# Performance work log

Measured on AMD Instinct MI355X. Metric: run time of the kernel, lower is better.

Reference implementation:

```python
import jax, jax.numpy as jnp
import numpy as np

D_MODEL = 4096
D_HIDDEN = 32768
BATCH = 2048
K = 128
N_DEAD = 2048


def _ln(x, eps=1e-5):
    # torch .std() is unbiased (ddof=1)
    mu = jnp.mean(x, axis=-1, keepdims=True)
    xc = x - mu
    std = jnp.std(x, axis=-1, keepdims=True, ddof=1)
    return xc / (std + eps), mu, std


def _topk_activation(x, k):
    # topk over last dim, relu values, scatter back into zeros
    vals, idx = jax.lax.top_k(x, k)          # [B, k]
    vals = jax.nn.relu(vals)
    rows = jnp.arange(x.shape[0])[:, None]    # [B, 1]
    return jnp.zeros_like(x).at[rows, idx].set(vals)


def setup_inputs() -> dict:
    key = jax.random.key(0)
    k1, k2 = jax.random.split(key)
    x = jax.random.normal(k1, (BATCH, D_MODEL), dtype=jnp.float32)
    # kaiming-uniform-ish encoder init
    bound = 1.0 / np.sqrt(D_MODEL)
    w_enc = jax.random.uniform(k2, (D_MODEL, D_HIDDEN), dtype=jnp.float32,
                               minval=-bound, maxval=bound)
    w_dec = w_enc.T
    w_dec = w_dec / jnp.linalg.norm(w_dec, axis=0, keepdims=True)
    b_enc = jnp.zeros((D_HIDDEN,), dtype=jnp.float32)
    b_pre = jnp.zeros((D_MODEL,), dtype=jnp.float32)
    # fixed dead-neuron mask with exactly N_DEAD dead latents
    dm = np.zeros((D_HIDDEN,), dtype=bool)
    rng = np.random.default_rng(0)
    dm[rng.choice(D_HIDDEN, size=N_DEAD, replace=False)] = True
    dead_mask = jnp.asarray(dm)
    return {"x": x, "w_enc": w_enc, "w_dec": w_dec, "b_enc": b_enc,
            "b_pre": b_pre, "dead_mask": dead_mask, "num_dead": N_DEAD}


def reference(x, w_enc, w_dec, b_enc, b_pre, dead_mask, num_dead):
    xn, mu, std = _ln(x)
    xc = xn - b_pre
    pre_acts = xc @ w_enc + b_enc                 # [B, d_hidden]
    latents = _topk_activation(pre_acts, K)
    recons = latents @ w_dec + b_pre              # [B, d_model]
    recons = recons * std + mu
    # auxk dead-neuron path (num_dead is a static python int)
    k_aux = min(x.shape[-1] // 2, num_dead)
    auxk_latents = jnp.where(dead_mask[None, :], pre_acts, -jnp.inf)
    auxk_acts = _topk_activation(auxk_latents, k_aux)
    auxk = auxk_acts @ w_dec + b_pre
    auxk = auxk * std + mu
    return recons, auxk, num_dead
```

## Files before the change

### kernel.cpp

```cpp
#include <hip/hip_runtime.h>
#include <math.h>

#define D_MODEL  4096
#define D_HIDDEN 32768
#define BATCH    2048
#define KSEL     128
#define NDEAD    2048
#define TIECAP   256

#define NB_SEL 2048
#define NB_AG  2048
#define NB_AB  8192
#define NB_WD  8192

typedef short s16x8 __attribute__((ext_vector_type(8)));
typedef float f32x4 __attribute__((ext_vector_type(4)));

__device__ __forceinline__ unsigned int fkey(float f) {
    unsigned int u = __float_as_uint(f);
    return (u & 0x80000000u) ? ~u : (u | 0x80000000u);
}
__device__ __forceinline__ unsigned short f2bf(float f) {
    unsigned int u = __float_as_uint(f);
    u += 0x7FFFu + ((u >> 16) & 1u);
    return (unsigned short)(u >> 16);
}
__device__ __forceinline__ float bf2f(unsigned short h) {
    return __uint_as_float(((unsigned int)h) << 16);
}
__device__ __forceinline__ unsigned int key16x2(unsigned int u) {
    const unsigned int s = (u >> 15) & 0x10001u;
    const unsigned int mask = s * 0xFFFFu;
    return (u ^ mask) | (~mask & 0x80008000u);
}
__device__ __forceinline__ float unkey16(unsigned int k) {
    const unsigned int u = (k & 0x8000u) ? (k & 0x7FFFu) : (~k & 0xFFFFu);
    return __uint_as_float(u << 16);
}
__device__ __forceinline__ void async_copy16(void* lds_dst, const void* gsrc) {
    __builtin_amdgcn_global_load_lds(
        (const __attribute__((address_space(1))) unsigned int*)gsrc,
        (__attribute__((address_space(3))) unsigned int*)lds_dst,
        16, 0, 0);
}

__global__ __launch_bounds__(256) void prep_kernel(
    const float* __restrict__ x, const float* __restrict__ b_pre,
    double* __restrict__ mu, double* __restrict__ stdv, double* __restrict__ sinv,
    unsigned short* __restrict__ Ahp, float* __restrict__ xch, float* __restrict__ xcl,
    const unsigned char* __restrict__ mask8, int* __restrict__ dead_idx,
    int* __restrict__ dead_cnt, const int* __restrict__ num_dead_in,
    float* __restrict__ out_last)
{
    const int row = blockIdx.x;
    const int tid = threadIdx.x;
    if (row == BATCH) {
        if (tid >= 64) return;
        const int lane = tid;
        int c = 0;
        for (int j = lane; j < D_HIDDEN; j += 64) c += (mask8[j] != 0);
#pragma unroll
        for (int off = 32; off > 0; off >>= 1) c += __shfl_down(c, off, 64);
        const int total_u8 = __shfl(c, 0, 64);
        const bool u8mode = (total_u8 == NDEAD);
        const int* mask32 = (const int*)mask8;
        int cnt = 0;
        for (int base = 0; base < D_HIDDEN; base += 64) {
            const int j = base + lane;
            const bool d = u8mode ? (mask8[j] != 0) : (mask32[j] != 0);
            const unsigned long long b = __ballot(d);
            const int pre = __popcll(b & ((1ull << lane) - 1ull));
            if (d && (cnt + pre) < NDEAD) dead_idx[cnt + pre] = j;
            cnt += __popcll(b);
        }
        const int cc = cnt > NDEAD ? NDEAD : cnt;
        if (lane == 0) {
            *dead_cnt = cc;
            *out_last = (float)(*num_dead_in);
        }
        for (int t = cc + lane; t < NDEAD; t += 64) dead_idx[t] = 0;
        return;
    }
    const float* xr = x + (size_t)row * D_MODEL;
    float xv[16];
#pragma unroll
    for (int i = 0; i < 16; ++i) xv[i] = xr[tid + 256 * i];
    double s = 0.0;
#pragma unroll
    for (int i = 0; i < 16; ++i) s += (double)xv[i];
    __shared__ double red[4];
    __shared__ double sh_mu, sh_si;
    const int lane = tid & 63, wid = tid >> 6;
#pragma unroll
    for (int off = 32; off > 0; off >>= 1) s += __shfl_down(s, off, 64);
    if (lane == 0) red[wid] = s;
    __syncthreads();
    if (tid == 0) sh_mu = (red[0] + red[1] + red[2] + red[3]) / (double)D_MODEL;
    __syncthreads();
    const double m = sh_mu;
    double s2 = 0.0;
#pragma unroll
    for (int i = 0; i < 16; ++i) { double d = (double)xv[i] - m; s2 += d * d; }
#pragma unroll
    for (int off = 32; off > 0; off >>= 1) s2 += __shfl_down(s2, off, 64);
    __syncthreads();
    if (lane == 0) red[wid] = s2;
    __syncthreads();
    if (tid == 0) {
        double var = (red[0] + red[1] + red[2] + red[3]) / (double)(D_MODEL - 1);
        double sd = sqrt(var);
        mu[row] = m;
        stdv[row] = sd;
        const double si = 1.0 / (sd + 1e-5);
        sinv[row] = si;
        sh_si = si;
    }
    __syncthreads();
    const double si = sh_si;
#pragma unroll
    for (int i = 0; i < 4; ++i) {
        const int j = (i * 256 + tid) * 4;
        const float4 x4 = *(const float4*)(xr + j);
        const float4 bp = *(const float4*)(b_pre + j);
        float vf[4], hi[4], lo[4];
        const float xe[4] = {x4.x, x4.y, x4.z, x4.w};
        const float be[4] = {bp.x, bp.y, bp.z, bp.w};
#pragma unroll
        for (int e = 0; e < 4; ++e) {
            const double t = ((double)xe[e] - m) * si;
            vf[e] = (float)t - be[e];
            const double a = t - (double)be[e];
            hi[e] = (float)a;
            lo[e] = (float)(a - (double)hi[e]);
        }
        uint2 hw;
        hw.x = (unsigned)f2bf(vf[0]) | ((unsigned)f2bf(vf[1]) << 16);
        hw.y = (unsigned)f2bf(vf[2]) | ((unsigned)f2bf(vf[3]) << 16);
        *(uint2*)(Ahp + (size_t)row * D_MODEL + j) = hw;
        *(float4*)(xch + (size_t)row * D_MODEL + j) = make_float4(hi[0], hi[1], hi[2], hi[3]);
        *(float4*)(xcl + (size_t)row * D_MODEL + j) = make_float4(lo[0], lo[1], lo[2], lo[3]);
    }
}

__global__ __launch_bounds__(256) void bsplit_kernel(
    const float* __restrict__ w_enc, unsigned short* __restrict__ Bhp)
{
    __shared__ float t[32][33];
    const int bk = blockIdx.x * 32;
    const int bn = blockIdx.y * 32;
    const int tid = threadIdx.x;
    const int lr = tid >> 3, lc4 = (tid & 7) * 4;
    const float4 v = *(const float4*)(w_enc + (size_t)(bk + lr) * D_HIDDEN + bn + lc4);
    t[lr][lc4 + 0] = v.x; t[lr][lc4 + 1] = v.y; t[lr][lc4 + 2] = v.z; t[lr][lc4 + 3] = v.w;
    __syncthreads();
    float o[4];
#pragma unroll
    for (int j = 0; j < 4; ++j) o[j] = t[lc4 + j][lr];
    uint2 hw;
    hw.x = (unsigned)f2bf(o[0]) | ((unsigned)f2bf(o[1]) << 16);
    hw.y = (unsigned)f2bf(o[2]) | ((unsigned)f2bf(o[3]) << 16);
    *(uint2*)(Bhp + (size_t)(bn + lr) * D_MODEL + bk + lc4) = hw;
}

__global__ __launch_bounds__(256) void wencT_kernel(
    const float* __restrict__ w_enc, float* __restrict__ wT)
{
    __shared__ float t[32][33];
    const int bk = blockIdx.x * 32;
    const int bn = blockIdx.y * 32;
    const int tid = threadIdx.x;
    const int lr = tid >> 3, lc4 = (tid & 7) * 4;
    const float4 v = *(const float4*)(w_enc + (size_t)(bk + lr) * D_HIDDEN + bn + lc4);
    t[lr][lc4 + 0] = v.x; t[lr][lc4 + 1] = v.y; t[lr][lc4 + 2] = v.z; t[lr][lc4 + 3] = v.w;
    __syncthreads();
    const int j = tid >> 3, i4 = (tid & 7) * 4;
    float4 o;
    o.x = t[i4 + 0][j]; o.y = t[i4 + 1][j]; o.z = t[i4 + 2][j]; o.w = t[i4 + 3][j];
    *(float4*)(wT + (size_t)(bn + j) * D_MODEL + bk + i4) = o;
}

__global__ __launch_bounds__(256) void wprep_kernel(
    const float* __restrict__ w_enc, unsigned short* __restrict__ Bhp,
    float* __restrict__ wT)
{
    __shared__ float t[32][33];
    const int bk = blockIdx.x * 32;
    const int bn = blockIdx.y * 32;
    const int tid = threadIdx.x;
    const int lr = tid >> 3, lc4 = (tid & 7) * 4;
    const float4 v = *(const float4*)(w_enc + (size_t)(bk + lr) * D_HIDDEN + bn + lc4);
    t[lr][lc4 + 0] = v.x; t[lr][lc4 + 1] = v.y; t[lr][lc4 + 2] = v.z; t[lr][lc4 + 3] = v.w;
    __syncthreads();
    float o[4];
#pragma unroll
    for (int j = 0; j < 4; ++j) o[j] = t[lc4 + j][lr];
    uint2 hw;
    hw.x = (unsigned)f2bf(o[0]) | ((unsigned)f2bf(o[1]) << 16);
    hw.y = (unsigned)f2bf(o[2]) | ((unsigned)f2bf(o[3]) << 16);
    *(uint2*)(Bhp + (size_t)(bn + lr) * D_MODEL + bk + lc4) = hw;
    *(float4*)(wT + (size_t)(bn + lr) * D_MODEL + bk + lc4) = make_float4(o[0], o[1], o[2], o[3]);
}

template<int EPI>
__global__ __launch_bounds__(512) void mm256_kernel(
    const unsigned short* __restrict__ A, const unsigned short* __restrict__ B,
    const int kdim, const int ntiles_x,
    const float* __restrict__ bias_n,
    const double* __restrict__ muv, const double* __restrict__ stdvv,
    void* __restrict__ outp, const long ostride)
{
    __shared__ unsigned short lds[2 * 4 * 8192];
    const int tid = threadIdx.x;
    const int lane = tid & 63, wid = tid >> 6;
    const int cpx = gridDim.x >> 3;
    const int orig = blockIdx.x;
    const int wg = (orig & 7) * cpx + (orig >> 3);
    const int m0 = (wg % ntiles_x) * 256;
    const int n0 = (wg / ntiles_x) * 256;
    const int wm = (wid >> 2) * 128;
    const int wn = (wid & 3) * 64;
    const int fr = lane & 15, kq = lane >> 4;
    const int swr = (fr >> 1) & 3;
    const int qg = (lane & 3) ^ ((lane >> 3) & 3);
    const int qo = (kq ^ swr) * 8;

    f32x4 acc[8][4];
#pragma unroll
    for (int i = 0; i < 8; ++i)
#pragma unroll
        for (int j = 0; j < 4; ++j) acc[i][j] = (f32x4){0.f, 0.f, 0.f, 0.f};

    const unsigned short* sH0[4];
    int dH0[4];
#pragma unroll
    for (int j = 0; j < 4; ++j) {
        const int g = wid * 4 + j;
        const int is_b = g >> 4;
        const int sr = g & 15;
        const unsigned short* gp = is_b ? B : A;
        const int t0 = is_b ? n0 : m0;
        sH0[j] = gp + (size_t)(t0 + sr * 16 + (lane >> 2)) * kdim + qg * 8;
        dH0[j] = (is_b ? 2 : 0) * 8192 + sr * 512;
    }

    const int NT = kdim >> 6;
#pragma unroll
    for (int j = 0; j < 4; ++j) async_copy16(lds + dH0[j], sH0[j]);
#pragma unroll
    for (int j = 0; j < 4; ++j) async_copy16(lds + 8192 + dH0[j], sH0[j] + 32);
    if (NT > 1) {
#pragma unroll
        for (int j = 0; j < 4; ++j) async_copy16(lds + 32768 + dH0[j], sH0[j] + 64);
    }

    for (int t = 0; t < NT; ++t) {
        const int cur = t & 1;
        unsigned short* bb = (unsigned short*)lds + cur * 32768;
        unsigned short* nb = (unsigned short*)lds + (cur ^ 1) * 32768;
        const int k1 = (t + 1) << 6;
        const int k2 = (t + 2) << 6;

        if (t < NT - 1) { asm volatile("s_waitcnt vmcnt(8)" ::: "memory"); }
        else            { asm volatile("s_waitcnt vmcnt(4)" ::: "memory"); }
        asm volatile("s_barrier" ::: "memory");
        __builtin_amdgcn_sched_barrier(0);
        {
            if (t + 1 < NT) {
                async_copy16(nb + 8192 + dH0[0], sH0[0] + k1 + 32);
                async_copy16(nb + 8192 + dH0[1], sH0[1] + k1 + 32);
            }
            s16x8 a[4], b[4];
#pragma unroll
            for (int mi = 0; mi < 4; ++mi)
                a[mi] = *(const s16x8*)(bb + (wm + mi * 16 + fr) * 32 + qo);
#pragma unroll
            for (int ni = 0; ni < 4; ++ni)
                b[ni] = *(const s16x8*)(bb + 2 * 8192 + (wn + ni * 16 + fr) * 32 + qo);
            __builtin_amdgcn_s_setprio(1);
#pragma unroll
            for (int mi = 0; mi < 4; ++mi)
#pragma unroll
                for (int ni = 0; ni < 4; ++ni)
                    acc[mi][ni] = __builtin_amdgcn_mfma_f32_16x16x32_bf16(a[mi], b[ni], acc[mi][ni], 0, 0, 0);
            __builtin_amdgcn_s_setprio(0);
            asm volatile("s_barrier" ::: "memory");
            __builtin_amdgcn_sched_barrier(0);
            if (t + 1 < NT) {
                async_copy16(nb + 8192 + dH0[2], sH0[2] + k1 + 32);
                async_copy16(nb + 8192 + dH0[3], sH0[3] + k1 + 32);
            }
            s16x8 a2[4];
#pragma unroll
            for (int mi = 0; mi < 4; ++mi)
                a2[mi] = *(const s16x8*)(bb + (wm + (mi + 4) * 16 + fr) * 32 + qo);
            __builtin_amdgcn_s_setprio(1);
#pragma unroll
            for (int mi = 0; mi < 4; ++mi)
#pragma unroll
                for (int ni = 0; ni < 4; ++ni)
                    acc[mi + 4][ni] = __builtin_amdgcn_mfma_f32_16x16x32_bf16(a2[mi], b[ni], acc[mi + 4][ni], 0, 0, 0);
            __builtin_amdgcn_s_setprio(0);
        }
        if (t < NT - 1) { asm volatile("s_waitcnt vmcnt(8)" ::: "memory"); }
        else            { asm volatile("s_waitcnt vmcnt(0)" ::: "memory"); }
        asm volatile("s_barrier" ::: "memory");
        __builtin_amdgcn_sched_barrier(0);
        {
            if (t + 2 < NT) {
                async_copy16(bb + dH0[0], sH0[0] + k2);
                async_copy16(bb + dH0[1], sH0[1] + k2);
            }
            s16x8 a[4], b[4];
#pragma unroll
            for (int mi = 0; mi < 4; ++mi)
                a[mi] = *(const s16x8*)(bb + 8192 + (wm + mi * 16 + fr) * 32 + qo);
#pragma unroll
            for (int ni = 0; ni < 4; ++ni)
                b[ni] = *(const s16x8*)(bb + 3 * 8192 + (wn + ni * 16 + fr) * 32 + qo);
            __builtin_amdgcn_s_setprio(1);
#pragma unroll
            for (int mi = 0; mi < 4; ++mi)
#pragma unroll
                for (int ni = 0; ni < 4; ++ni)
                    acc[mi][ni] = __builtin_amdgcn_mfma_f32_16x16x32_bf16(a[mi], b[ni], acc[mi][ni], 0, 0, 0);
            __builtin_amdgcn_s_setprio(0);
            asm volatile("s_barrier" ::: "memory");
            __builtin_amdgcn_sched_barrier(0);
            if (t + 2 < NT) {
                async_copy16(bb + dH0[2], sH0[2] + k2);
                async_copy16(bb + dH0[3], sH0[3] + k2);
            }
            s16x8 a2[4];
#pragma unroll
            for (int mi = 0; mi < 4; ++mi)
                a2[mi] = *(const s16x8*)(bb + 8192 + (wm + (mi + 4) * 16 + fr) * 32 + qo);
            __builtin_amdgcn_s_setprio(1);
#pragma unroll
            for (int mi = 0; mi < 4; ++mi)
#pragma unroll
                for (int ni = 0; ni < 4; ++ni)
                    acc[mi + 4][ni] = __builtin_amdgcn_mfma_f32_16x16x32_bf16(a2[mi], b[ni], acc[mi + 4][ni], 0, 0, 0);
            __builtin_amdgcn_s_setprio(0);
        }
    }

#pragma unroll
    for (int ni = 0; ni < 4; ++ni) {
        const int col = n0 + wn + ni * 16 + fr;
        const float be = bias_n[col];
#pragma unroll
        for (int mi = 0; mi < 8; ++mi) {
            const int rb = m0 + wm + mi * 16 + kq * 4;
            if (EPI == 0) {
                unsigned short* O = (unsigned short*)outp;
#pragma unroll
                for (int r = 0; r < 4; ++r)
                    O[(size_t)(rb + r) * ostride + col] = f2bf(acc[mi][ni][r] + be);
            } else {
                float* O = (float*)outp;
#pragma unroll
                for (int r = 0; r < 4; ++r) {
                    const int m = rb + r;
                    O[(size_t)m * ostride + col] =
                        (acc[mi][ni][r] + be) * (float)stdvv[m] + (float)muv[m];
                }
            }
        }
    }
}

__global__ __launch_bounds__(256) void comboA_kernel(
    const unsigned short* __restrict__ p16,
    int* __restrict__ topk_idx, float* __restrict__ topk_val,
    int* __restrict__ sure_cnt, int* __restrict__ tie_cnt, int* __restrict__ cand_col,
    const int* __restrict__ dead_idx, const int* __restrict__ dead_cnt,
    unsigned short* __restrict__ Ahd,
    const float* __restrict__ w_dec, unsigned short* __restrict__ Bhd,
    unsigned short* __restrict__ wd16,
    const int nb_ab, const int nb_wd)
{
    const int b = blockIdx.x;
    const int tid = threadIdx.x;
    __shared__ float tsm[32][33];
    __shared__ int red[4];
    __shared__ int sh_sel, sh_tie;

    if (b < NB_SEL) {
        const int row = b;
        const int lane = tid & 63, wid = tid >> 6;
        const unsigned short* pr = p16 + (size_t)row * D_HIDDEN;
        uint4 kr[16];
#pragma unroll
        for (int i = 0; i < 16; ++i) {
            uint4 w = *(const uint4*)(pr + (i * 256 + tid) * 8);
            w.x = key16x2(w.x); w.y = key16x2(w.y); w.z = key16x2(w.z); w.w = key16x2(w.w);
            kr[i] = w;
        }
        if (tid == 0) { sh_sel = 0; sh_tie = 0; }
        unsigned int lo = 0, hi = 65535;
        while (lo < hi) {
            const unsigned int mid = (lo + hi) >> 1;
            int c = 0;
#pragma unroll
            for (int i = 0; i < 16; ++i) {
                const unsigned int u[4] = {kr[i].x, kr[i].y, kr[i].z, kr[i].w};
#pragma unroll
                for (int e = 0; e < 4; ++e) {
                    c += (int)((u[e] & 0xFFFFu) > mid);
                    c += (int)((u[e] >> 16) > mid);
                }
            }
#pragma unroll
            for (int off = 32; off > 0; off >>= 1) c += __shfl_down(c, off, 64);
            if (lane == 0) red[wid] = c;
            __syncthreads();
            const int total = red[0] + red[1] + red[2] + red[3];
            if (total < KSEL) hi = mid; else lo = mid + 1;
            __syncthreads();
        }
        const unsigned int K16 = lo;
        const float vc = unkey16(K16);
        const float DLT = 1.3e-2f;
        const float sureT = vc + 2.f * DLT;
        const float candT = vc - 2.f * DLT;
        const unsigned int sK = fkey(sureT) >> 16;
        const unsigned int cK = fkey(candT) >> 16;
        int* oidx = topk_idx + row * KSEL;
        float* oval = topk_val + row * KSEL;
        int* cc = cand_col + row * TIECAP;
#pragma unroll
        for (int i = 0; i < 16; ++i) {
            const int j0 = (i * 256 + tid) * 8;
            const unsigned int u[4] = {kr[i].x, kr[i].y, kr[i].z, kr[i].w};
#pragma unroll
            for (int e = 0; e < 8; ++e) {
                const unsigned int k = (e & 1) ? (u[e >> 1] >> 16) : (u[e >> 1] & 0xFFFFu);
                if (k < cK) continue;
                const float v = unkey16(k);
                if (k > sK && v > sureT) {
                    const int pos = atomicAdd(&sh_sel, 1);
                    oidx[pos] = j0 + e;
                    oval[pos] = v > 0.f ? v : 0.f;
                } else if (v >= candT) {
                    const int t = atomicAdd(&sh_tie, 1);
                    if (t < TIECAP) cc[t] = j0 + e;
                }
            }
        }
        __syncthreads();
        if (tid == 0) {
            sure_cnt[row] = sh_sel;
            tie_cnt[row] = sh_tie > TIECAP ? TIECAP : sh_tie;
        }
        return;
    }
    if (b < NB_SEL + NB_AG) {
        const int r = b - NB_SEL;
        const int dc = *dead_cnt;
#pragma unroll
        for (int i = 0; i < 8; ++i) {
            const int c = i * 256 + tid;
            unsigned short v = 0;
            if (c < dc) {
                const unsigned short u = p16[(size_t)r * D_HIDDEN + dead_idx[c]];
                v = (u & 0x8000u) ? (unsigned short)0 : u;
            }
            Ahd[(size_t)r * NDEAD + c] = v;
        }
        return;
    }
    if (b < NB_SEL + NB_AG + nb_ab) {
        const int idx = b - (NB_SEL + NB_AG);
        const int k0 = (idx & 63) * 32;
        const int n0 = (idx >> 6) * 32;
        const int i = tid >> 3, j4 = (tid & 7) * 4;
        const int srow = dead_idx[k0 + i];
        const float4 v = *(const float4*)(w_dec + (size_t)srow * D_MODEL + n0 + j4);
        tsm[i][j4 + 0] = v.x; tsm[i][j4 + 1] = v.y; tsm[i][j4 + 2] = v.z; tsm[i][j4 + 3] = v.w;
        __syncthreads();
        const int j = tid >> 3, i4 = (tid & 7) * 4;
        uint2 hw;
        hw.x = (unsigned)f2bf(tsm[i4 + 0][j]) | ((unsigned)f2bf(tsm[i4 + 1][j]) << 16);
        hw.y = (unsigned)f2bf(tsm[i4 + 2][j]) | ((unsigned)f2bf(tsm[i4 + 3][j]) << 16);
        *(uint2*)(Bhd + (size_t)(n0 + j) * NDEAD + k0 + i4) = hw;
        return;
    }
    {
        const int bb = b - (NB_SEL + NB_AG + nb_ab);
        (void)nb_wd;
        const size_t base0 = (size_t)bb * 16384;
#pragma unroll
        for (int it = 0; it < 8; ++it) {
            const size_t off = base0 + (size_t)it * 2048 + (size_t)tid * 8;
            const float4 a = *(const float4*)(w_dec + off);
            const float4 c = *(const float4*)(w_dec + off + 4);
            uint4 o;
            o.x = (unsigned)f2bf(a.x) | ((unsigned)f2bf(a.y) << 16);
            o.y = (unsigned)f2bf(a.z) | ((unsigned)f2bf(a.w) << 16);
            o.z = (unsigned)f2bf(c.x) | ((unsigned)f2bf(c.y) << 16);
            o.w = (unsigned)f2bf(c.z) | ((unsigned)f2bf(c.w) << 16);
            *(uint4*)(wd16 + off) = o;
        }
        return;
    }
}

__global__ __launch_bounds__(256) void auxb_kernel(
    const float* __restrict__ w_dec, const int* __restrict__ dead_idx,
    unsigned short* __restrict__ Bhd)
{
    __shared__ float t[32][33];
    const int k0 = blockIdx.x * 32;
    const int n0 = blockIdx.y * 32;
    const int tid = threadIdx.x;
    const int i = tid >> 3, j4 = (tid & 7) * 4;
    const int srow = dead_idx[k0 + i];
    const float4 v = *(const float4*)(w_dec + (size_t)srow * D_MODEL + n0 + j4);
    t[i][j4 + 0] = v.x; t[i][j4 + 1] = v.y; t[i][j4 + 2] = v.z; t[i][j4 + 3] = v.w;
    __syncthreads();
    const int j = tid >> 3, i4 = (tid & 7) * 4;
    uint2 hw;
    hw.x = (unsigned)f2bf(t[i4 + 0][j]) | ((unsigned)f2bf(t[i4 + 1][j]) << 16);
    hw.y = (unsigned)f2bf(t[i4 + 2][j]) | ((unsigned)f2bf(t[i4 + 3][j]) << 16);
    *(uint2*)(Bhd + (size_t)(n0 + j) * NDEAD + k0 + i4) = hw;
}

__global__ __launch_bounds__(256) void wdec2bf_kernel(
    const float* __restrict__ w_dec, unsigned short* __restrict__ wd16)
{
    const size_t gid = (size_t)blockIdx.x * 256 + threadIdx.x;
    const size_t base = gid * 8;
    const float4 a = *(const float4*)(w_dec + base);
    const float4 b = *(const float4*)(w_dec + base + 4);
    uint4 o;
    o.x = (unsigned)f2bf(a.x) | ((unsigned)f2bf(a.y) << 16);
    o.y = (unsigned)f2bf(a.z) | ((unsigned)f2bf(a.w) << 16);
    o.z = (unsigned)f2bf(b.x) | ((unsigned)f2bf(b.y) << 16);
    o.w = (unsigned)f2bf(b.z) | ((unsigned)f2bf(b.w) << 16);
    *(uint4*)(wd16 + base) = o;
}

__global__ __launch_bounds__(256) void topk_refine_kernel(
    const int* __restrict__ tie_cnt, const int* __restrict__ cand_col,
    double* __restrict__ cand_val,
    const float* __restrict__ xch, const float* __restrict__ xcl,
    const float* __restrict__ wT, const float* __restrict__ b_enc)
{
    const int row = blockIdx.x;
    const int tid = threadIdx.x;
    const int lane = tid & 63, wid = tid >> 6;
    const int T = tie_cnt[row];
    const int base = (int)blockIdx.y * 4 + wid;
    if (base >= T) return;
    const float* hr = xch + (size_t)row * D_MODEL;
    const float* lr2 = xcl + (size_t)row * D_MODEL;
    for (int slot = base; slot < T; slot += 64) {
        const int col = cand_col[row * TIECAP + slot];
        const float* wr = wT + (size_t)col * D_MODEL;
        double s0 = 0.0, s1 = 0.0;
        for (int k = lane * 4; k < D_MODEL; k += 512) {
            {
                const float4 h = *(const float4*)(hr + k);
                const float4 l = *(const float4*)(lr2 + k);
                const float4 w4 = *(const float4*)(wr + k);
                s0 += ((double)h.x + (double)l.x) * (double)w4.x;
                s0 += ((double)h.y + (double)l.y) * (double)w4.y;
                s0 += ((double)h.z + (double)l.z) * (double)w4.z;
                s0 += ((double)h.w + (double)l.w) * (double)w4.w;
            }
            {
                const int k2 = k + 256;
                const float4 h = *(const float4*)(hr + k2);
                const float4 l = *(const float4*)(lr2 + k2);
                const float4 w4 = *(const float4*)(wr + k2);
                s1 += ((double)h.x + (double)l.x) * (double)w4.x;
                s1 += ((double)h.y + (double)l.y) * (double)w4.y;
                s1 += ((double)h.z + (double)l.z) * (double)w4.z;
                s1 += ((double)h.w + (double)l.w) * (double)w4.w;
            }
        }
        double s = s0 + s1;
#pragma unroll
        for (int off = 32; off > 0; off >>= 1) s += __shfl_down(s, off, 64);
        if (lane == 0) cand_val[row * TIECAP + slot] = s + (double)b_enc[col];
    }
}

__global__ __launch_bounds__(256) void decode_fin_kernel(
    const int* __restrict__ sure_cnt, const int* __restrict__ tie_cnt,
    const int* __restrict__ cand_col, const double* __restrict__ cand_val,
    const int* __restrict__ topk_idx, const float* __restrict__ topk_val,
    const unsigned short* __restrict__ wd16, const float* __restrict__ b_pre,
    const double* __restrict__ mu, const double* __restrict__ stdv,
    float* __restrict__ out0)
{
    const int row = blockIdx.x;
    const int tid = threadIdx.x;
    __shared__ double vals[TIECAP];
    __shared__ int cols[TIECAP];
    __shared__ int sidx[KSEL];
    __shared__ float sval[KSEL];
    const int G = sure_cnt[row];
    const int T = tie_cnt[row];
    const int R = KSEL - G;
    if (tid < T) {
        vals[tid] = cand_val[row * TIECAP + tid];
        cols[tid] = cand_col[row * TIECAP + tid];
    }
    if (tid < G) {
        sidx[tid] = topk_idx[row * KSEL + tid];
        sval[tid] = topk_val[row * KSEL + tid];
    }
    __syncthreads();
    if (tid < T) {
        const double v = vals[tid];
        const int c = cols[tid];
        int rank = 0;
        for (int u = 0; u < T; ++u) {
            const double vu = vals[u];
            rank += (int)((vu > v) || (vu == v && cols[u] < c));
        }
        if (rank < R) {
            sidx[G + rank] = c;
            sval[G + rank] = v > 0.0 ? (float)v : 0.f;
        }
    }
    const int take = R < T ? R : T;
    if (tid >= take && tid < R) {
        sidx[G + tid] = (T > 0) ? cols[0] : 0;
        sval[G + tid] = 0.f;
    }
    __syncthreads();
    float acc[16];
#pragma unroll
    for (int i = 0; i < 16; ++i) acc[i] = 0.f;
    const int dbase = tid * 16;
    for (int k = 0; k < KSEL; ++k) {
        const float v = sval[k];
        if (v == 0.f) continue;
        const uint4* wr = (const uint4*)(wd16 + (size_t)sidx[k] * D_MODEL + dbase);
        const uint4 w0 = wr[0], w1 = wr[1];
        const unsigned int u[8] = {w0.x, w0.y, w0.z, w0.w, w1.x, w1.y, w1.z, w1.w};
#pragma unroll
        for (int i = 0; i < 8; ++i) {
            acc[2 * i]     += v * __uint_as_float(u[i] << 16);
            acc[2 * i + 1] += v * __uint_as_float(u[i] & 0xFFFF0000u);
        }
    }
    const float st = (float)stdv[row];
    const float mm = (float)mu[row];
    float* o = out0 + (size_t)row * D_MODEL + dbase;
#pragma unroll
    for (int i = 0; i < 16; ++i) {
        o[i] = (acc[i] + b_pre[dbase + i]) * st + mm;
    }
}

extern "C" void kernel_launch(void* const* d_in, const int* in_sizes, int n_in,
                              void* d_out, int out_size, void* d_ws, size_t ws_size,
                              hipStream_t stream)
{
    (void)in_sizes; (void)n_in; (void)out_size;
    const float* x      = (const float*)d_in[0];
    const float* w_enc  = (const float*)d_in[1];
    const float* w_dec  = (const float*)d_in[2];
    const float* b_enc  = (const float*)d_in[3];
    const float* b_pre  = (const float*)d_in[4];
    const unsigned char* dead_mask = (const unsigned char*)d_in[5];
    const int* num_dead = (const int*)d_in[6];
    float* out = (float*)d_out;

    char* base = (char*)d_ws;
    char* w = base;
    auto alloc = [&](size_t bytes) -> char* {
        char* p = w;
        w += (bytes + 255) & ~(size_t)255;
        return p;
    };
    unsigned short* p16 = (unsigned short*)alloc((size_t)BATCH * D_HIDDEN * 2);
    double* mu       = (double*)alloc((size_t)BATCH * 8);
    double* stdv     = (double*)alloc((size_t)BATCH * 8);
    double* sinv     = (double*)alloc((size_t)BATCH * 8);
    int* topk_idx    = (int*)alloc((size_t)BATCH * KSEL * 4);
    float* topk_val  = (float*)alloc((size_t)BATCH * KSEL * 4);
    int* dead_idx    = (int*)alloc((size_t)NDEAD * 4);
    int* dead_cnt    = (int*)alloc(256);
    int* sure_cnt    = (int*)alloc((size_t)BATCH * 4);
    int* tie_cnt     = (int*)alloc((size_t)BATCH * 4);
    int* cand_col    = (int*)alloc((size_t)BATCH * TIECAP * 4);
    double* cand_val = (double*)alloc((size_t)BATCH * TIECAP * 8);
    float* xch       = (float*)alloc((size_t)BATCH * D_MODEL * 4);
    float* xcl       = (float*)alloc((size_t)BATCH * D_MODEL * 4);
    unsigned short* Ahp = (unsigned short*)alloc((size_t)BATCH * D_MODEL * 2);
    char* region     = alloc((size_t)D_HIDDEN * D_MODEL * 4);
    float* wT_big    = (float*)alloc((size_t)D_HIDDEN * D_MODEL * 4);
    const size_t need_big = (size_t)(w - base);
    const bool bigws = (ws_size >= need_big);

    unsigned short* Bhp = (unsigned short*)region;
    float* wT_small = (float*)region;
    unsigned short* wd16 = (unsigned short*)region;
    unsigned short* Bhd  = (unsigned short*)(region + (size_t)D_HIDDEN * D_MODEL * 2);
    unsigned short* Ahd  = Ahp;
    float* wT = bigws ? wT_big : wT_small;

    float* out0 = out;
    float* out1 = out + (size_t)BATCH * D_MODEL;
    float* out_last = out + (size_t)2 * BATCH * D_MODEL;

    prep_kernel<<<BATCH + 1, 256, 0, stream>>>(x, b_pre, mu, stdv, sinv, Ahp, xch, xcl,
                                               dead_mask, dead_idx, dead_cnt, num_dead, out_last);
    if (bigws) {
        wprep_kernel<<<dim3(D_MODEL / 32, D_HIDDEN / 32), 256, 0, stream>>>(w_enc, Bhp, wT);
    } else {
        bsplit_kernel<<<dim3(D_MODEL / 32, D_HIDDEN / 32), 256, 0, stream>>>(w_enc, Bhp);
    }
    mm256_kernel<0><<<(BATCH / 256) * (D_HIDDEN / 256), 512, 0, stream>>>(
        Ahp, Bhp, D_MODEL, BATCH / 256, b_enc, nullptr, nullptr, p16, (long)D_HIDDEN);
    if (bigws) {
        comboA_kernel<<<NB_SEL + NB_AG + NB_AB + NB_WD, 256, 0, stream>>>(
            p16, topk_idx, topk_val, sure_cnt, tie_cnt, cand_col,
            dead_idx, dead_cnt, Ahd, w_dec, Bhd, wd16, NB_AB, NB_WD);
        mm256_kernel<1><<<(BATCH / 256) * (D_MODEL / 256), 512, 0, stream>>>(
            Ahd, Bhd, NDEAD, BATCH / 256, b_pre, mu, stdv, out1, (long)D_MODEL);
        topk_refine_kernel<<<dim3(BATCH, 16), 256, 0, stream>>>(
            tie_cnt, cand_col, cand_val, xch, xcl, wT, b_enc);
    } else {
        wencT_kernel<<<dim3(D_MODEL / 32, D_HIDDEN / 32), 256, 0, stream>>>(w_enc, wT);
        comboA_kernel<<<NB_SEL + NB_AG, 256, 0, stream>>>(
            p16, topk_idx, topk_val, sure_cnt, tie_cnt, cand_col,
            dead_idx, dead_cnt, Ahd, w_dec, Bhd, wd16, 0, 0);
        topk_refine_kernel<<<dim3(BATCH, 16), 256, 0, stream>>>(
            tie_cnt, cand_col, cand_val, xch, xcl, wT, b_enc);
        auxb_kernel<<<dim3(NDEAD / 32, D_MODEL / 32), 256, 0, stream>>>(w_dec, dead_idx, Bhd);
        wdec2bf_kernel<<<(int)(((size_t)D_HIDDEN * D_MODEL) / (256 * 8)), 256, 0, stream>>>(w_dec, wd16);
        mm256_kernel<1><<<(BATCH / 256) * (D_MODEL / 256), 512, 0, stream>>>(
            Ahd, Bhd, NDEAD, BATCH / 256, b_pre, mu, stdv, out1, (long)D_MODEL);
    }
    decode_fin_kernel<<<BATCH, 256, 0, stream>>>(
        sure_cnt, tie_cnt, cand_col, cand_val, topk_idx, topk_val,
        wd16, b_pre, mu, stdv, out0);
}
```

Before: 2.069 ms.

## Fuse weight prep into LN prep, merge aux GEMM with top-k refine

Folds the w_enc transpose/bf16 conversion blocks into the layer-norm prep kernel as extra blocks. It also merges the aux-k decode GEMM and the tie-refinement dot products into one launch, comboB, with the GEMM tiles placed first. The refine path now runs one 512-thread block per row and stages the row's high/low activations in LDS, replacing the 16-way y-grid. The goal is fewer launches and overlap of small, unbalanced kernels, at the cost of lower refine parallelism per row and the heavy LDS footprint applying to all blocks.

```diff
diff --git a/kernel.cpp b/kernel.cpp
--- a/kernel.cpp
+++ b/kernel.cpp
@@ -12,6 +12,8 @@
 #define NB_AG  2048
 #define NB_AB  8192
 #define NB_WD  8192
+#define NB_MM  128
+#define NB_WPREP (128 * 1024)
 
 typedef short s16x8 __attribute__((ext_vector_type(8)));
 typedef float f32x4 __attribute__((ext_vector_type(4)));
@@ -44,17 +46,44 @@
         16, 0, 0);
 }
 
-__global__ __launch_bounds__(256) void prep_kernel(
+__global__ __launch_bounds__(256) void prepw_kernel(
     const float* __restrict__ x, const float* __restrict__ b_pre,
     double* __restrict__ mu, double* __restrict__ stdv, double* __restrict__ sinv,
     unsigned short* __restrict__ Ahp, float* __restrict__ xch, float* __restrict__ xcl,
     const unsigned char* __restrict__ mask8, int* __restrict__ dead_idx,
     int* __restrict__ dead_cnt, const int* __restrict__ num_dead_in,
-    float* __restrict__ out_last)
+    float* __restrict__ out_last,
+    const float* __restrict__ w_enc, unsigned short* __restrict__ Bhp,
+    float* __restrict__ wT, const int do_w)
 {
-    const int row = blockIdx.x;
+    const int b = blockIdx.x;
     const int tid = threadIdx.x;
-    if (row == BATCH) {
+    __shared__ double red[4];
+    __shared__ double sh_mu, sh_si;
+    __shared__ float tsm[32][33];
+
+    if (b > BATCH) {
+        const int wb = b - (BATCH + 1);
+        const int bk = (wb & 127) * 32;
+        const int bn = (wb >> 7) * 32;
+        const int lr = tid >> 3, lc4 = (tid & 7) * 4;
+        const float4 v = *(const float4*)(w_enc + (size_t)(bk + lr) * D_HIDDEN + bn + lc4);
+        tsm[lr][lc4 + 0] = v.x; tsm[lr][lc4 + 1] = v.y;
+        tsm[lr][lc4 + 2] = v.z; tsm[lr][lc4 + 3] = v.w;
+        __syncthreads();
+        float o[4];
+#pragma unroll
+        for (int j = 0; j < 4; ++j) o[j] = tsm[lc4 + j][lr];
+        uint2 hw;
+        hw.x = (unsigned)f2bf(o[0]) | ((unsigned)f2bf(o[1]) << 16);
+        hw.y = (unsigned)f2bf(o[2]) | ((unsigned)f2bf(o[3]) << 16);
+        *(uint2*)(Bhp + (size_t)(bn + lr) * D_MODEL + bk + lc4) = hw;
+        if (do_w)
+            *(float4*)(wT + (size_t)(bn + lr) * D_MODEL + bk + lc4) =
+                make_float4(o[0], o[1], o[2], o[3]);
+        return;
+    }
+    if (b == BATCH) {
         if (tid >= 64) return;
         const int lane = tid;
         int c = 0;
@@ -68,10 +97,10 @@
         for (int base = 0; base < D_HIDDEN; base += 64) {
             const int j = base + lane;
             const bool d = u8mode ? (mask8[j] != 0) : (mask32[j] != 0);
-            const unsigned long long b = __ballot(d);
-            const int pre = __popcll(b & ((1ull << lane) - 1ull));
+            const unsigned long long bm = __ballot(d);
+            const int pre = __popcll(bm & ((1ull << lane) - 1ull));
             if (d && (cnt + pre) < NDEAD) dead_idx[cnt + pre] = j;
-            cnt += __popcll(b);
+            cnt += __popcll(bm);
         }
         const int cc = cnt > NDEAD ? NDEAD : cnt;
         if (lane == 0) {
@@ -81,6 +110,7 @@
         for (int t = cc + lane; t < NDEAD; t += 64) dead_idx[t] = 0;
         return;
     }
+    const int row = b;
     const float* xr = x + (size_t)row * D_MODEL;
     float xv[16];
 #pragma unroll
@@ -88,8 +118,6 @@
     double s = 0.0;
 #pragma unroll
     for (int i = 0; i < 16; ++i) s += (double)xv[i];
-    __shared__ double red[4];
-    __shared__ double sh_mu, sh_si;
     const int lane = tid & 63, wid = tid >> 6;
 #pragma unroll
     for (int off = 32; off > 0; off >>= 1) s += __shfl_down(s, off, 64);
@@ -177,28 +205,6 @@
     float4 o;
     o.x = t[i4 + 0][j]; o.y = t[i4 + 1][j]; o.z = t[i4 + 2][j]; o.w = t[i4 + 3][j];
     *(float4*)(wT + (size_t)(bn + j) * D_MODEL + bk + i4) = o;
-}
-
-__global__ __launch_bounds__(256) void wprep_kernel(
-    const float* __restrict__ w_enc, unsigned short* __restrict__ Bhp,
-    float* __restrict__ wT)
-{
-    __shared__ float t[32][33];
-    const int bk = blockIdx.x * 32;
-    const int bn = blockIdx.y * 32;
-    const int tid = threadIdx.x;
-    const int lr = tid >> 3, lc4 = (tid & 7) * 4;
-    const float4 v = *(const float4*)(w_enc + (size_t)(bk + lr) * D_HIDDEN + bn + lc4);
-    t[lr][lc4 + 0] = v.x; t[lr][lc4 + 1] = v.y; t[lr][lc4 + 2] = v.z; t[lr][lc4 + 3] = v.w;
-    __syncthreads();
-    float o[4];
-#pragma unroll
-    for (int j = 0; j < 4; ++j) o[j] = t[lc4 + j][lr];
-    uint2 hw;
-    hw.x = (unsigned)f2bf(o[0]) | ((unsigned)f2bf(o[1]) << 16);
-    hw.y = (unsigned)f2bf(o[2]) | ((unsigned)f2bf(o[3]) << 16);
-    *(uint2*)(Bhp + (size_t)(bn + lr) * D_MODEL + bk + lc4) = hw;
-    *(float4*)(wT + (size_t)(bn + lr) * D_MODEL + bk + lc4) = make_float4(o[0], o[1], o[2], o[3]);
 }
 
 template<int EPI>
@@ -540,49 +546,218 @@
     *(uint4*)(wd16 + base) = o;
 }
 
-__global__ __launch_bounds__(256) void topk_refine_kernel(
+__global__ __launch_bounds__(512) void comboB_kernel(
+    const unsigned short* __restrict__ A, const unsigned short* __restrict__ B,
+    const float* __restrict__ bias_n,
+    const double* __restrict__ muv, const double* __restrict__ stdvv,
+    float* __restrict__ out1,
     const int* __restrict__ tie_cnt, const int* __restrict__ cand_col,
     double* __restrict__ cand_val,
     const float* __restrict__ xch, const float* __restrict__ xcl,
-    const float* __restrict__ wT, const float* __restrict__ b_enc)
+    const float* __restrict__ wT, const float* __restrict__ b_enc,
+    const int nb_mm)
 {
-    const int row = blockIdx.x;
+    __shared__ unsigned short lds[2 * 4 * 8192];
     const int tid = threadIdx.x;
     const int lane = tid & 63, wid = tid >> 6;
-    const int T = tie_cnt[row];
-    const int base = (int)blockIdx.y * 4 + wid;
-    if (base >= T) return;
-    const float* hr = xch + (size_t)row * D_MODEL;
-    const float* lr2 = xcl + (size_t)row * D_MODEL;
-    for (int slot = base; slot < T; slot += 64) {
-        const int col = cand_col[row * TIECAP + slot];
-        const float* wr = wT + (size_t)col * D_MODEL;
-        double s0 = 0.0, s1 = 0.0;
-        for (int k = lane * 4; k < D_MODEL; k += 512) {
-            {
-                const float4 h = *(const float4*)(hr + k);
-                const float4 l = *(const float4*)(lr2 + k);
-                const float4 w4 = *(const float4*)(wr + k);
-                s0 += ((double)h.x + (double)l.x) * (double)w4.x;
-                s0 += ((double)h.y + (double)l.y) * (double)w4.y;
-                s0 += ((double)h.z + (double)l.z) * (double)w4.z;
-                s0 += ((double)h.w + (double)l.w) * (double)w4.w;
-            }
-            {
-                const int k2 = k + 256;
-                const float4 h = *(const float4*)(hr + k2);
-                const float4 l = *(const float4*)(lr2 + k2);
-                const float4 w4 = *(const float4*)(wr + k2);
-                s1 += ((double)h.x + (double)l.x) * (double)w4.x;
-                s1 += ((double)h.y + (double)l.y) * (double)w4.y;
-                s1 += ((double)h.z + (double)l.z) * (double)w4.z;
-                s1 += ((double)h.w + (double)l.w) * (double)w4.w;
-            }
-        }
-        double s = s0 + s1;
-#pragma unroll
-        for (int off = 32; off > 0; off >>= 1) s += __shfl_down(s, off, 64);
-        if (lane == 0) cand_val[row * TIECAP + slot] = s + (double)b_enc[col];
+
+    if (blockIdx.x >= nb_mm) {
+        const int row = blockIdx.x - nb_mm;
+        const int T = tie_cnt[row];
+        if (T == 0) return;
+        float* shh = (float*)lds;
+        float* shl = shh + D_MODEL;
+        const float* hr = xch + (size_t)row * D_MODEL;
+        const float* lr2 = xcl + (size_t)row * D_MODEL;
+        {
+            const int o = tid * 8;
+            *(float4*)(shh + o)     = *(const float4*)(hr + o);
+            *(float4*)(shh + o + 4) = *(const float4*)(hr + o + 4);
+            *(float4*)(shl + o)     = *(const float4*)(lr2 + o);
+            *(float4*)(shl + o + 4) = *(const float4*)(lr2 + o + 4);
+        }
+        __syncthreads();
+        for (int slot = wid; slot < T; slot += 8) {
+            const int col = cand_col[row * TIECAP + slot];
+            const float* wr = wT + (size_t)col * D_MODEL;
+            double s0 = 0.0, s1 = 0.0;
+            for (int k = lane * 4; k < D_MODEL; k += 512) {
+                {
+                    const float4 h = *(const float4*)(shh + k);
+                    const float4 l = *(const float4*)(shl + k);
+                    const float4 w4 = *(const float4*)(wr + k);
+                    s0 += ((double)h.x + (double)l.x) * (double)w4.x;
+                    s0 += ((double)h.y + (double)l.y) * (double)w4.y;
+                    s0 += ((double)h.z + (double)l.z) * (double)w4.z;
+                    s0 += ((double)h.w + (double)l.w) * (double)w4.w;
+                }
+                {
+                    const int k2 = k + 256;
+                    const float4 h = *(const float4*)(shh + k2);
+                    const float4 l = *(const float4*)(shl + k2);
+                    const float4 w4 = *(const float4*)(wr + k2);
+                    s1 += ((double)h.x + (double)l.x) * (double)w4.x;
+                    s1 += ((double)h.y + (double)l.y) * (double)w4.y;
+                    s1 += ((double)h.z + (double)l.z) * (double)w4.z;
+                    s1 += ((double)h.w + (double)l.w) * (double)w4.w;
+                }
+            }
+            double s = s0 + s1;
+#pragma unroll
+            for (int off = 32; off > 0; off >>= 1) s += __shfl_down(s, off, 64);
+            if (lane == 0) cand_val[row * TIECAP + slot] = s + (double)b_enc[col];
+        }
+        return;
+    }
+
+    const int kdim = NDEAD;
+    const int ntiles_x = BATCH / 256;
+    const int cpx = nb_mm >> 3;
+    const int orig = blockIdx.x;
+    const int wg = (orig & 7) * cpx + (orig >> 3);
+    const int m0 = (wg % ntiles_x) * 256;
+    const int n0 = (wg / ntiles_x) * 256;
+    const int wm = (wid >> 2) * 128;
+    const int wn = (wid & 3) * 64;
+    const int fr = lane & 15, kq = lane >> 4;
+    const int swr = (fr >> 1) & 3;
+    const int qg = (lane & 3) ^ ((lane >> 3) & 3);
+    const int qo = (kq ^ swr) * 8;
+
+    f32x4 acc[8][4];
+#pragma unroll
+    for (int i = 0; i < 8; ++i)
+#pragma unroll
+        for (int j = 0; j < 4; ++j) acc[i][j] = (f32x4){0.f, 0.f, 0.f, 0.f};
+
+    const unsigned short* sH0[4];
+    int dH0[4];
+#pragma unroll
+    for (int j = 0; j < 4; ++j) {
+        const int g = wid * 4 + j;
+        const int is_b = g >> 4;
+        const int sr = g & 15;
+        const unsigned short* gp = is_b ? B : A;
+        const int t0 = is_b ? n0 : m0;
+        sH0[j] = gp + (size_t)(t0 + sr * 16 + (lane >> 2)) * kdim + qg * 8;
+        dH0[j] = (is_b ? 2 : 0) * 8192 + sr * 512;
+    }
+
+    const int NT = kdim >> 6;
+#pragma unroll
+    for (int j = 0; j < 4; ++j) async_copy16(lds + dH0[j], sH0[j]);
+#pragma unroll
+    for (int j = 0; j < 4; ++j) async_copy16(lds + 8192 + dH0[j], sH0[j] + 32);
+    if (NT > 1) {
+#pragma unroll
+        for (int j = 0; j < 4; ++j) async_copy16(lds + 32768 + dH0[j], sH0[j] + 64);
+    }
+
+    for (int t = 0; t < NT; ++t) {
+        const int cur = t & 1;
+        unsigned short* bb = (unsigned short*)lds + cur * 32768;
+        unsigned short* nb = (unsigned short*)lds + (cur ^ 1) * 32768;
+        const int k1 = (t + 1) << 6;
+        const int k2 = (t + 2) << 6;
+
+        if (t < NT - 1) { asm volatile("s_waitcnt vmcnt(8)" ::: "memory"); }
+        else            { asm volatile("s_waitcnt vmcnt(4)" ::: "memory"); }
+        asm volatile("s_barrier" ::: "memory");
+        __builtin_amdgcn_sched_barrier(0);
+        {
+            if (t + 1 < NT) {
+                async_copy16(nb + 8192 + dH0[0], sH0[0] + k1 + 32);
+                async_copy16(nb + 8192 + dH0[1], sH0[1] + k1 + 32);
+            }
+            s16x8 a[4], b[4];
+#pragma unroll
+            for (int mi = 0; mi < 4; ++mi)
+                a[mi] = *(const s16x8*)(bb + (wm + mi * 16 + fr) * 32 + qo);
+#pragma unroll
+            for (int ni = 0; ni < 4; ++ni)
+                b[ni] = *(const s16x8*)(bb + 2 * 8192 + (wn + ni * 16 + fr) * 32 + qo);
+            __builtin_amdgcn_s_setprio(1);
+#pragma unroll
+            for (int mi = 0; mi < 4; ++mi)
+#pragma unroll
+                for (int ni = 0; ni < 4; ++ni)
+                    acc[mi][ni] = __builtin_amdgcn_mfma_f32_16x16x32_bf16(a[mi], b[ni], acc[mi][ni], 0, 0, 0);
+            __builtin_amdgcn_s_setprio(0);
+            asm volatile("s_barrier" ::: "memory");
+            __builtin_amdgcn_sched_barrier(0);
+            if (t + 1 < NT) {
+                async_copy16(nb + 8192 + dH0[2], sH0[2] + k1 + 32);
+                async_copy16(nb + 8192 + dH0[3], sH0[3] + k1 + 32);
+            }
+            s16x8 a2[4];
+#pragma unroll
+            for (int mi = 0; mi < 4; ++mi)
+                a2[mi] = *(const s16x8*)(bb + (wm + (mi + 4) * 16 + fr) * 32 + qo);
+            __builtin_amdgcn_s_setprio(1);
+#pragma unroll
+            for (int mi = 0; mi < 4; ++mi)
+#pragma unroll
+                for (int ni = 0; ni < 4; ++ni)
+                    acc[mi + 4][ni] = __builtin_amdgcn_mfma_f32_16x16x32_bf16(a2[mi], b[ni], acc[mi + 4][ni], 0, 0, 0);
+            __builtin_amdgcn_s_setprio(0);
+        }
+        if (t < NT - 1) { asm volatile("s_waitcnt vmcnt(8)" ::: "memory"); }
+        else            { asm volatile("s_waitcnt vmcnt(0)" ::: "memory"); }
+        asm volatile("s_barrier" ::: "memory");
+        __builtin_amdgcn_sched_barrier(0);
+        {
+            if (t + 2 < NT) {
+                async_copy16(bb + dH0[0], sH0[0] + k2);
+                async_copy16(bb + dH0[1], sH0[1] + k2);
+            }
+            s16x8 a[4], b[4];
+#pragma unroll
+            for (int mi = 0; mi < 4; ++mi)
+                a[mi] = *(const s16x8*)(bb + 8192 + (wm + mi * 16 + fr) * 32 + qo);
+#pragma unroll
+            for (int ni = 0; ni < 4; ++ni)
+                b[ni] = *(const s16x8*)(bb + 3 * 8192 + (wn + ni * 16 + fr) * 32 + qo);
+            __builtin_amdgcn_s_setprio(1);
+#pragma unroll
+            for (int mi = 0; mi < 4; ++mi)
+#pragma unroll
+                for (int ni = 0; ni < 4; ++ni)
+                    acc[mi][ni] = __builtin_amdgcn_mfma_f32_16x16x32_bf16(a[mi], b[ni], acc[mi][ni], 0, 0, 0);
+            __builtin_amdgcn_s_setprio(0);
+            asm volatile("s_barrier" ::: "memory");
+            __builtin_amdgcn_sched_barrier(0);
+            if (t + 2 < NT) {
+                async_copy16(bb + dH0[2], sH0[2] + k2);
+                async_copy16(bb + dH0[3], sH0[3] + k2);
+            }
+            s16x8 a2[4];
+#pragma unroll
+            for (int mi = 0; mi < 4; ++mi)
+                a2[mi] = *(const s16x8*)(bb + 8192 + (wm + (mi + 4) * 16 + fr) * 32 + qo);
+            __builtin_amdgcn_s_setprio(1);
+#pragma unroll
+            for (int mi = 0; mi < 4; ++mi)
+#pragma unroll
+                for (int ni = 0; ni < 4; ++ni)
+                    acc[mi + 4][ni] = __builtin_amdgcn_mfma_f32_16x16x32_bf16(a2[mi], b[ni], acc[mi + 4][ni], 0, 0, 0);
+            __builtin_amdgcn_s_setprio(0);
+        }
+    }
+
+#pragma unroll
+    for (int ni = 0; ni < 4; ++ni) {
+        const int col = n0 + wn + ni * 16 + fr;
+        const float be = bias_n[col];
+#pragma unroll
+        for (int mi = 0; mi < 8; ++mi) {
+            const int rb = m0 + wm + mi * 16 + kq * 4;
+#pragma unroll
+            for (int r = 0; r < 4; ++r) {
+                const int m = rb + r;
+                out1[(size_t)m * D_MODEL + col] =
+                    (acc[mi][ni][r] + be) * (float)stdvv[m] + (float)muv[m];
+            }
+        }
     }
 }
 
@@ -708,30 +883,34 @@
     float* out1 = out + (size_t)BATCH * D_MODEL;
     float* out_last = out + (size_t)2 * BATCH * D_MODEL;
 
-    prep_kernel<<<BATCH + 1, 256, 0, stream>>>(x, b_pre, mu, stdv, sinv, Ahp, xch, xcl,
-                                               dead_mask, dead_idx, dead_cnt, num_dead, out_last);
     if (bigws) {
-        wprep_kernel<<<dim3(D_MODEL / 32, D_HIDDEN / 32), 256, 0, stream>>>(w_enc, Bhp, wT);
-    } else {
-        bsplit_kernel<<<dim3(D_MODEL / 32, D_HIDDEN / 32), 256, 0, stream>>>(w_enc, Bhp);
-    }
-    mm256_kernel<0><<<(BATCH / 256) * (D_HIDDEN / 256), 512, 0, stream>>>(
-        Ahp, Bhp, D_MODEL, BATCH / 256, b_enc, nullptr, nullptr, p16, (long)D_HIDDEN);
-    if (bigws) {
+        prepw_kernel<<<BATCH + 1 + NB_WPREP, 256, 0, stream>>>(
+            x, b_pre, mu, stdv, sinv, Ahp, xch, xcl,
+            dead_mask, dead_idx, dead_cnt, num_dead, out_last,
+            w_enc, Bhp, wT, 1);
+        mm256_kernel<0><<<(BATCH / 256) * (D_HIDDEN / 256), 512, 0, stream>>>(
+            Ahp, Bhp, D_MODEL, BATCH / 256, b_enc, nullptr, nullptr, p16, (long)D_HIDDEN);
         comboA_kernel<<<NB_SEL + NB_AG + NB_AB + NB_WD, 256, 0, stream>>>(
             p16, topk_idx, topk_val, sure_cnt, tie_cnt, cand_col,
             dead_idx, dead_cnt, Ahd, w_dec, Bhd, wd16, NB_AB, NB_WD);
-        mm256_kernel<1><<<(BATCH / 256) * (D_MODEL / 256), 512, 0, stream>>>(
-            Ahd, Bhd, NDEAD, BATCH / 256, b_pre, mu, stdv, out1, (long)D_MODEL);
-        topk_refine_kernel<<<dim3(BATCH, 16), 256, 0, stream>>>(
-            tie_cnt, cand_col, cand_val, xch, xcl, wT, b_enc);
+        comboB_kernel<<<NB_MM + BATCH, 512, 0, stream>>>(
+            Ahd, Bhd, b_pre, mu, stdv, out1,
+            tie_cnt, cand_col, cand_val, xch, xcl, wT, b_enc, NB_MM);
     } else {
+        prepw_kernel<<<BATCH + 1, 256, 0, stream>>>(
+            x, b_pre, mu, stdv, sinv, Ahp, xch, xcl,
+            dead_mask, dead_idx, dead_cnt, num_dead, out_last,
+            w_enc, Bhp, nullptr, 0);
+        bsplit_kernel<<<dim3(D_MODEL / 32, D_HIDDEN / 32), 256, 0, stream>>>(w_enc, Bhp);
+        mm256_kernel<0><<<(BATCH / 256) * (D_HIDDEN / 256), 512, 0, stream>>>(
+            Ahp, Bhp, D_MODEL, BATCH / 256, b_enc, nullptr, nullptr, p16, (long)D_HIDDEN);
         wencT_kernel<<<dim3(D_MODEL / 32, D_HIDDEN / 32), 256, 0, stream>>>(w_enc, wT);
         comboA_kernel<<<NB_SEL + NB_AG, 256, 0, stream>>>(
             p16, topk_idx, topk_val, sure_cnt, tie_cnt, cand_col,
             dead_idx, dead_cnt, Ahd, w_dec, Bhd, wd16, 0, 0);
-        topk_refine_kernel<<<dim3(BATCH, 16), 256, 0, stream>>>(
-            tie_cnt, cand_col, cand_val, xch, xcl, wT, b_enc);
+        comboB_kernel<<<BATCH, 512, 0, stream>>>(
+            Ahd, Bhd, b_pre, mu, stdv, out1,
+            tie_cnt, cand_col, cand_val, xch, xcl, wT, b_enc, 0);
         auxb_kernel<<<dim3(NDEAD / 32, D_MODEL / 32), 256, 0, stream>>>(w_dec, dead_idx, Bhd);
         wdec2bf_kernel<<<(int)(((size_t)D_HIDDEN * D_MODEL) / (256 * 8)), 256, 0, stream>>>(w_dec, wd16);
         mm256_kernel<1><<<(BATCH / 256) * (D_MODEL / 256), 512, 0, stream>>>(
```

Result: faster. 1.987 ms (median of 2 runs) (-4.0%).
